# Kernel tuning notes

Hardware: AMD Instinct MI355X
Metric: run time of the kernel (lower is better)

Reference implementation:

```python
import jax, jax.numpy as jnp
import numpy as np

D, H, KVH, HD, FF = 768, 12, 4, 64, 2048
N_REP = H // KVH
EPS = 1e-6


def rmsnorm(x, w):
    # Faithful to source: norm = ||x|| * n^{-1/2}; eps added to norm (not inside sqrt)
    norm = jnp.sqrt(jnp.sum(x * x, axis=-1, keepdims=True)) * (x.shape[-1] ** -0.5)
    return w * x / (norm + EPS)


def rope_tables(seq_len, head_dim, base=10000.0):
    inv_freq = 1.0 / (base ** (np.arange(0, head_dim, 2, dtype=np.float32) / head_dim))
    t = np.arange(seq_len, dtype=np.float32)
    freqs = np.einsum('i,j->ij', t, inv_freq)  # [S, HD/2]
    emb = np.concatenate([freqs, freqs], axis=-1)  # [S, HD]
    return jnp.asarray(np.cos(emb)), jnp.asarray(np.sin(emb))


def rotate_half(x):
    h = x.shape[-1] // 2
    return jnp.concatenate([-x[..., h:], x[..., :h]], axis=-1)


def setup_inputs() -> dict:
    key = jax.random.key(0)
    ks = jax.random.split(key, 9)
    s = 0.02
    return {
        'x': jax.random.normal(ks[0], (2, 2048, D), jnp.float32),
        'Wq': jax.random.normal(ks[1], (H * HD, D), jnp.float32) * s,
        'Wk': jax.random.normal(ks[2], (KVH * HD, D), jnp.float32) * s,
        'Wv': jax.random.normal(ks[3], (KVH * HD, D), jnp.float32) * s,
        'Wo': jax.random.normal(ks[4], (D, H * HD), jnp.float32) * s,
        'Wgate': jax.random.normal(ks[5], (FF, D), jnp.float32) * s,
        'Wup': jax.random.normal(ks[6], (FF, D), jnp.float32) * s,
        'Wdown': jax.random.normal(ks[7], (D, FF), jnp.float32) * s,
        'g1': jnp.ones((D,), jnp.float32),
        'g2': jnp.ones((D,), jnp.float32),
    }


def reference(x, Wq, Wk, Wv, Wo, Wgate, Wup, Wdown, g1, g2):
    B, S, _ = x.shape
    # ---- attention sublayer (pre-norm) ----
    xn = rmsnorm(x, g1)
    q = (xn @ Wq.T).reshape(B, S, H, HD).transpose(0, 2, 1, 3)      # [B,H,S,HD]
    k = (xn @ Wk.T).reshape(B, S, KVH, HD).transpose(0, 2, 1, 3)    # [B,KVH,S,HD]
    v = (xn @ Wv.T).reshape(B, S, KVH, HD).transpose(0, 2, 1, 3)
    cos, sin = rope_tables(S, HD)                                   # [S,HD]
    q = q * cos + rotate_half(q) * sin
    k = k * cos + rotate_half(k) * sin
    # repeat kv heads to match q heads
    k = jnp.repeat(k, N_REP, axis=1)                                # [B,H,S,HD]
    v = jnp.repeat(v, N_REP, axis=1)
    scores = jnp.einsum('bhqd,bhkd->bhqk', q, k) / jnp.sqrt(jnp.float32(HD))
    causal = jnp.tril(jnp.ones((S, S), bool))
    scores = jnp.where(causal, scores, jnp.finfo(scores.dtype).min)
    attn = jax.nn.softmax(scores, axis=-1)
    out = jnp.einsum('bhqk,bhkd->bhqd', attn, v)                    # [B,H,S,HD]
    out = out.transpose(0, 2, 1, 3).reshape(B, S, H * HD) @ Wo.T
    x = x + out
    # ---- SwiGLU FFN sublayer (pre-norm) ----
    xn2 = rmsnorm(x, g2)
    ff = (jax.nn.silu(xn2 @ Wgate.T) * (xn2 @ Wup.T)) @ Wdown.T
    return x + ff
```

## Files before the change

### kernel.cpp

```cpp
#include <hip/hip_runtime.h>
#include <hip/hip_bf16.h>
#include <math.h>

typedef __bf16 bf16;
typedef __attribute__((ext_vector_type(8))) __bf16 bf16x8;
typedef __attribute__((ext_vector_type(4))) __bf16 bf16x4;
typedef __attribute__((ext_vector_type(4))) float f32x4;

#define MFMA16(a,b,c) __builtin_amdgcn_mfma_f32_16x16x32_bf16(a,b,c,0,0,0)

#define BATCH 2
#define SEQ   2048
#define DMODEL 768
#define NH    12
#define NKV   4
#define NREP  3
#define HD    64
#define FFDIM 2048
#define ROWS  (BATCH*SEQ)

#define QSCALE 0.18033688011112042f
#define LOG2E  1.4426950408889634f

#define WB(N) asm volatile("s_waitcnt vmcnt(" #N ")\n\ts_barrier" ::: "memory")
#define BAR() asm volatile("s_barrier" ::: "memory")

__device__ __forceinline__ void gl2lds16(const bf16* g, bf16* l) {
  __builtin_amdgcn_global_load_lds(
      (const __attribute__((address_space(1))) void*)g,
      (__attribute__((address_space(3))) void*)l, 16, 0, 0);
}

struct Cvt7 { const float* s[7]; bf16* d[7]; int n[7]; };
__global__ __launch_bounds__(256) void cvt_all_kernel(Cvt7 c) {
  int seg = blockIdx.y;
  const float* __restrict__ src = c.s[seg];
  bf16* __restrict__ dst = c.d[seg];
  int n = c.n[seg];
  int stride = gridDim.x * 256;
  for (int i = blockIdx.x * 256 + threadIdx.x; i < n; i += stride)
    dst[i] = (bf16)src[i];
}

__global__ __launch_bounds__(256) void rope_tab_kernel(float* __restrict__ tab) {
  int id = blockIdx.x * 256 + threadIdx.x;
  int j = id >> 11, s = id & 2047;
  float inv = expf(-(float)j * (9.210340371976184f / 32.0f));
  float ang = (float)s * inv;
  tab[id] = cosf(ang);
  tab[65536 + id] = sinf(ang);
}

__global__ __launch_bounds__(192) void rmsnorm_kernel(const float* __restrict__ x,
    const float* __restrict__ g, bf16* __restrict__ out) {
  int row = blockIdx.x;
  const float* xr = x + (size_t)row * DMODEL;
  int t = threadIdx.x;
  f32x4 v = *(const f32x4*)(xr + t * 4);
  float ss = v[0] * v[0] + v[1] * v[1] + v[2] * v[2] + v[3] * v[3];
  #pragma unroll
  for (int off = 32; off; off >>= 1) ss += __shfl_xor(ss, off, 64);
  __shared__ float red[3];
  if ((t & 63) == 0) red[t >> 6] = ss;
  __syncthreads();
  float total = red[0] + red[1] + red[2];
  float norm = sqrtf(total) * 0.03608439182435161f;
  float sc = 1.0f / (norm + 1e-6f);
  f32x4 gv = *(const f32x4*)(g + t * 4);
  bf16x4 o;
  #pragma unroll
  for (int i = 0; i < 4; ++i) o[i] = (bf16)(gv[i] * v[i] * sc);
  *(bf16x4*)(out + (size_t)row * DMODEL + t * 4) = o;
}

__global__ __launch_bounds__(256) void gemm_pipe64_kernel(const bf16* __restrict__ A,
    const bf16* __restrict__ B, float* __restrict__ C, const float* __restrict__ R,
    int N, int K) {
  __shared__ __align__(16) bf16 At[4][64 * 32];
  __shared__ __align__(16) bf16 Bt[4][64 * 32];
  int t = threadIdx.x, lane = t & 63, wave = t >> 6;
  int l15 = lane & 15, lq = lane >> 4;
  int wrow = (wave >> 1) * 32, wcol = (wave & 1) * 32;
  int row0 = blockIdx.y * 64, col0 = blockIdx.x * 64;
  const bf16* Ag = A + (size_t)(row0 + (t >> 2)) * K + (t & 3) * 8;
  const bf16* Bg = B + (size_t)(col0 + (t >> 2)) * K + (t & 3) * 8;
  const int NS = K / 32;

  #pragma unroll
  for (int s = 0; s < 4; ++s) {
    int ks = s * 32;
    gl2lds16(Ag + ks, At[s] + t * 8);
    gl2lds16(Bg + ks, Bt[s] + t * 8);
  }

  f32x4 zero = {0.f, 0.f, 0.f, 0.f};
  f32x4 acc[2][2];
  #pragma unroll
  for (int m = 0; m < 2; ++m)
    #pragma unroll
    for (int n = 0; n < 2; ++n) acc[m][n] = zero;

  #define GP_COMPUTE(slot) do {                                              \
    const bf16* at = At[slot]; const bf16* bt = Bt[slot];                    \
    bf16x8 af[2], bfr[2];                                                    \
    _Pragma("unroll")                                                        \
    for (int m = 0; m < 2; ++m)                                              \
      af[m] = *(const bf16x8*)(at + (wrow + m * 16 + l15) * 32 + lq * 8);    \
    _Pragma("unroll")                                                        \
    for (int n = 0; n < 2; ++n)                                              \
      bfr[n] = *(const bf16x8*)(bt + (wcol + n * 16 + l15) * 32 + lq * 8);   \
    _Pragma("unroll")                                                        \
    for (int m = 0; m < 2; ++m)                                              \
      _Pragma("unroll")                                                      \
      for (int n = 0; n < 2; ++n)                                            \
        acc[m][n] = MFMA16(af[m], bfr[n], acc[m][n]);                        \
  } while (0)

  for (int k = 0; k < NS - 3; ++k) {
    WB(6);
    GP_COMPUTE(k & 3);
    BAR();
    if (k <= NS - 5) {
      int ks = (k + 4) * 32;
      gl2lds16(Ag + ks, At[k & 3] + t * 8);
      gl2lds16(Bg + ks, Bt[k & 3] + t * 8);
    }
  }
  for (int k = NS - 3; k < NS; ++k) {
    WB(0);
    GP_COMPUTE(k & 3);
  }
  #undef GP_COMPUTE

  #pragma unroll
  for (int m = 0; m < 2; ++m)
    #pragma unroll
    for (int n = 0; n < 2; ++n)
      #pragma unroll
      for (int r = 0; r < 4; ++r) {
        size_t idx = (size_t)(row0 + wrow + m * 16 + lq * 4 + r) * N
                   + (col0 + wcol + n * 16 + l15);
        C[idx] = acc[m][n][r] + R[idx];
      }
}

__global__ __launch_bounds__(256) void gemm_qkv_kernel(const bf16* __restrict__ A,
    const bf16* __restrict__ Wcat, const float* __restrict__ tab,
    bf16* __restrict__ Qh, bf16* __restrict__ Kh, bf16* __restrict__ Vt) {
  __shared__ __align__(16) bf16 At[4][64 * 32];
  __shared__ __align__(16) bf16 Bt[4][128 * 32];
  const int K = DMODEL;
  int t = threadIdx.x, lane = t & 63, wave = t >> 6;
  int l15 = lane & 15, lq = lane >> 4;
  int wrow = (wave >> 1) * 32, wcol = (wave & 1) * 64;
  int row0 = blockIdx.y * 64, col0 = blockIdx.x * 128;
  const bf16* Ag  = A + (size_t)(row0 + (t >> 2)) * K + (t & 3) * 8;
  const bf16* Bg0 = Wcat + (size_t)(col0 + (t >> 2)) * K + (t & 3) * 8;
  const bf16* Bg1 = Bg0 + (size_t)64 * K;
  const int NS = K / 32;

  #pragma unroll
  for (int s = 0; s < 4; ++s) {
    int ks = s * 32;
    gl2lds16(Ag + ks,  At[s] + t * 8);
    gl2lds16(Bg0 + ks, Bt[s] + t * 8);
    gl2lds16(Bg1 + ks, Bt[s] + 2048 + t * 8);
  }

  f32x4 zero = {0.f, 0.f, 0.f, 0.f};
  f32x4 acc[2][4];
  #pragma unroll
  for (int m = 0; m < 2; ++m)
    #pragma unroll
    for (int n = 0; n < 4; ++n) acc[m][n] = zero;

  #define QK_COMPUTE(slot) do {                                              \
    const bf16* at = At[slot]; const bf16* bt = Bt[slot];                    \
    bf16x8 af[2], bfr[4];                                                    \
    _Pragma("unroll")                                                        \
    for (int m = 0; m < 2; ++m)                                              \
      af[m] = *(const bf16x8*)(at + (wrow + m * 16 + l15) * 32 + lq * 8);    \
    _Pragma("unroll")                                                        \
    for (int n = 0; n < 4; ++n)                                              \
      bfr[n] = *(const bf16x8*)(bt + (wcol + n * 16 + l15) * 32 + lq * 8);   \
    _Pragma("unroll")                                                        \
    for (int m = 0; m < 2; ++m)                                              \
      _Pragma("unroll")                                                      \
      for (int n = 0; n < 4; ++n)                                            \
        acc[m][n] = MFMA16(af[m], bfr[n], acc[m][n]);                        \
  } while (0)

  for (int k = 0; k < NS - 3; ++k) {
    WB(9);
    QK_COMPUTE(k & 3);
    BAR();
    if (k <= NS - 5) {
      int ks = (k + 4) * 32;
      gl2lds16(Ag + ks,  At[k & 3] + t * 8);
      gl2lds16(Bg0 + ks, Bt[k & 3] + t * 8);
      gl2lds16(Bg1 + ks, Bt[k & 3] + 2048 + t * 8);
    }
  }
  for (int k = NS - 3; k < NS; ++k) {
    WB(0);
    QK_COMPUTE(k & 3);
  }
  #undef QK_COMPUTE

  int b = row0 >> 11;
  int s0 = (row0 & 2047) + wrow + lq * 4;
  int colw = col0 + wcol;
  if (colw < 768) {
    int h = colw >> 6;
    f32x4 cv[2][2], sv[2][2];
    #pragma unroll
    for (int m = 0; m < 2; ++m)
      #pragma unroll
      for (int jh = 0; jh < 2; ++jh) {
        const float* cp = tab + (jh * 16 + l15) * 2048 + s0 + m * 16;
        cv[m][jh] = *(const f32x4*)cp;
        sv[m][jh] = *(const f32x4*)(cp + 65536);
      }
    #pragma unroll
    for (int m = 0; m < 2; ++m)
      #pragma unroll
      for (int n = 0; n < 4; ++n) {
        float sgn = (n < 2) ? -1.f : 1.f;
        #pragma unroll
        for (int r = 0; r < 4; ++r) {
          float c = cv[m][n & 1][r], si = sv[m][n & 1][r];
          float rp = (acc[m][n][r] * c + sgn * acc[m][n ^ 2][r] * si) * QSCALE;
          Qh[((size_t)(b * NH + h) * SEQ + s0 + m * 16 + r) * 64 + n * 16 + l15] = (bf16)rp;
        }
      }
  } else if (colw < 1024) {
    int kh = (colw - 768) >> 6;
    f32x4 cv[2][2], sv[2][2];
    #pragma unroll
    for (int m = 0; m < 2; ++m)
      #pragma unroll
      for (int jh = 0; jh < 2; ++jh) {
        const float* cp = tab + (jh * 16 + l15) * 2048 + s0 + m * 16;
        cv[m][jh] = *(const f32x4*)cp;
        sv[m][jh] = *(const f32x4*)(cp + 65536);
      }
    #pragma unroll
    for (int m = 0; m < 2; ++m)
      #pragma unroll
      for (int n = 0; n < 4; ++n) {
        float sgn = (n < 2) ? -1.f : 1.f;
        #pragma unroll
        for (int r = 0; r < 4; ++r) {
          float c = cv[m][n & 1][r], si = sv[m][n & 1][r];
          float rp = acc[m][n][r] * c + sgn * acc[m][n ^ 2][r] * si;
          Kh[((size_t)(b * NKV + kh) * SEQ + s0 + m * 16 + r) * 64 + n * 16 + l15] = (bf16)rp;
        }
      }
  } else {
    int vh = (colw - 1024) >> 6;
    #pragma unroll
    for (int m = 0; m < 2; ++m)
      #pragma unroll
      for (int n = 0; n < 4; ++n) {
        bf16x4 pv;
        #pragma unroll
        for (int r = 0; r < 4; ++r) pv[r] = (bf16)acc[m][n][r];
        *(bf16x4*)(Vt + ((size_t)(b * NKV + vh) * 64 + n * 16 + l15) * SEQ + s0 + m * 16) = pv;
      }
  }
}

__global__ __launch_bounds__(256) void gemm_gu_kernel(const bf16* __restrict__ A,
    const bf16* __restrict__ Wg, const bf16* __restrict__ Wu, bf16* __restrict__ H) {
  __shared__ __align__(16) bf16 At[3][128 * 32];
  __shared__ __align__(16) bf16 Bgt[3][64 * 32];
  __shared__ __align__(16) bf16 But[3][64 * 32];
  const int K = DMODEL;
  int t = threadIdx.x, lane = t & 63, wave = t >> 6;
  int l15 = lane & 15, lq = lane >> 4;
  int wrow = (wave >> 1) * 64, wcol = (wave & 1) * 32;
  int row0 = blockIdx.y * 128, col0 = blockIdx.x * 64;
  const bf16* Ag0 = A + (size_t)(row0 + (t >> 2)) * K + (t & 3) * 8;
  const bf16* Ag1 = Ag0 + (size_t)64 * K;
  const bf16* Gg  = Wg + (size_t)(col0 + (t >> 2)) * K + (t & 3) * 8;
  const bf16* Ug  = Wu + (size_t)(col0 + (t >> 2)) * K + (t & 3) * 8;
  const int NS = K / 32;

  #pragma unroll
  for (int s = 0; s < 3; ++s) {
    int ks = s * 32;
    gl2lds16(Ag0 + ks, At[s] + t * 8);
    gl2lds16(Ag1 + ks, At[s] + 2048 + t * 8);
    gl2lds16(Gg + ks,  Bgt[s] + t * 8);
    gl2lds16(Ug + ks,  But[s] + t * 8);
  }

  f32x4 zero = {0.f, 0.f, 0.f, 0.f};
  f32x4 ag[4][2], au[4][2];
  #pragma unroll
  for (int m = 0; m < 4; ++m)
    #pragma unroll
    for (int n = 0; n < 2; ++n) { ag[m][n] = zero; au[m][n] = zero; }

  #define GU_COMPUTE(slot) do {                                              \
    const bf16* at = At[slot];                                               \
    const bf16* bgt = Bgt[slot]; const bf16* but = But[slot];                \
    bf16x8 af[4], bg[2], bu[2];                                              \
    _Pragma("unroll")                                                        \
    for (int m = 0; m < 4; ++m)                                              \
      af[m] = *(const bf16x8*)(at + (wrow + m * 16 + l15) * 32 + lq * 8);    \
    _Pragma("unroll")                                                        \
    for (int n = 0; n < 2; ++n) {                                            \
      bg[n] = *(const bf16x8*)(bgt + (wcol + n * 16 + l15) * 32 + lq * 8);   \
      bu[n] = *(const bf16x8*)(but + (wcol + n * 16 + l15) * 32 + lq * 8);   \
    }                                                                        \
    _Pragma("unroll")                                                        \
    for (int m = 0; m < 4; ++m)                                              \
      _Pragma("unroll")                                                      \
      for (int n = 0; n < 2; ++n) {                                          \
        ag[m][n] = MFMA16(af[m], bg[n], ag[m][n]);                           \
        au[m][n] = MFMA16(af[m], bu[n], au[m][n]);                           \
      }                                                                      \
  } while (0)

  int slot = 0;
  for (int k = 0; k < NS - 2; ++k) {
    WB(8);
    GU_COMPUTE(slot);
    BAR();
    if (k <= NS - 4) {
      int ks = (k + 3) * 32;
      gl2lds16(Ag0 + ks, At[slot] + t * 8);
      gl2lds16(Ag1 + ks, At[slot] + 2048 + t * 8);
      gl2lds16(Gg + ks,  Bgt[slot] + t * 8);
      gl2lds16(Ug + ks,  But[slot] + t * 8);
    }
    slot = (slot == 2) ? 0 : slot + 1;
  }
  for (int k = NS - 2; k < NS; ++k) {
    WB(0);
    GU_COMPUTE(slot);
    slot = (slot == 2) ? 0 : slot + 1;
  }
  #undef GU_COMPUTE

  #pragma unroll
  for (int m = 0; m < 4; ++m)
    #pragma unroll
    for (int n = 0; n < 2; ++n)
      #pragma unroll
      for (int r = 0; r < 4; ++r) {
        int row = row0 + wrow + m * 16 + lq * 4 + r;
        int col = col0 + wcol + n * 16 + l15;
        float g = ag[m][n][r], u = au[m][n][r];
        float sg = g / (1.f + __builtin_amdgcn_exp2f(-g * LOG2E));
        H[(size_t)row * FFDIM + col] = (bf16)(sg * u);
      }
}

__global__ __launch_bounds__(256) void attn_kernel(const bf16* __restrict__ Qh,
    const bf16* __restrict__ Kh, const bf16* __restrict__ Vt, bf16* __restrict__ out) {
  __shared__ __align__(16) bf16 Kl0[2][64 * 32];
  __shared__ __align__(16) bf16 Kl1[2][64 * 32];
  __shared__ __align__(16) bf16 Vl0[2][64 * 32];
  __shared__ __align__(16) bf16 Vl1[2][64 * 32];
  __shared__ __align__(16) bf16 P[4][16 * 80];

  int idx = blockIdx.x;
  int qt = 31 - (idx / 24);
  int bh = idx % 24;
  int q0blk = qt * 64;
  int b = bh / NH, h = bh % NH;
  int kvh = h / NREP;
  int t = threadIdx.x;
  int lane = t & 63, wave = t >> 6;
  int l15 = lane & 15, lq = lane >> 4;
  int qw = q0blk + wave * 16;
  const bf16* Qb = Qh + (size_t)(b * NH + h) * SEQ * 64;
  const bf16* Kb = Kh + (size_t)(b * NKV + kvh) * SEQ * 64;
  const bf16* Vb = Vt + (size_t)(b * NKV + kvh) * 64 * SEQ;

  bf16x8 bq0 = *(const bf16x8*)(Qb + (size_t)(qw + l15) * 64 + lq * 8);
  bf16x8 bq1 = *(const bf16x8*)(Qb + (size_t)(qw + l15) * 64 + 32 + lq * 8);

  const bf16* Kg = Kb + (size_t)(t >> 2) * 64 + (t & 3) * 8;
  const bf16* Vg = Vb + (size_t)(t >> 2) * SEQ + (t & 3) * 8;
  bf16* Pw = P[wave];
  int Pwq = l15 * 80, lq8 = lq * 8, lq4 = lq * 4;
  const int NS = qt + 1;

  #pragma unroll
  for (int s = 0; s < 2; ++s) {
    int ks = (s < NS ? s : NS - 1) * 64;
    gl2lds16(Kg + (size_t)ks * 64,      Kl0[s] + t * 8);
    gl2lds16(Kg + (size_t)ks * 64 + 32, Kl1[s] + t * 8);
    gl2lds16(Vg + ks,                   Vl0[s] + t * 8);
    gl2lds16(Vg + ks + 32,              Vl1[s] + t * 8);
  }

  f32x4 zero = {0.f, 0.f, 0.f, 0.f};
  f32x4 o[4];
  o[0] = zero; o[1] = zero; o[2] = zero; o[3] = zero;
  float l_r = 0.f;

  #define ATTN_STEP(kk, slot) do {                                           \
    int k0 = (kk) * 64;                                                      \
    const bf16* kl0 = Kl0[slot]; const bf16* kl1 = Kl1[slot];                \
    const bf16* vl0 = Vl0[slot]; const bf16* vl1 = Vl1[slot];                \
    f32x4 s[4];                                                              \
    _Pragma("unroll")                                                        \
    for (int c = 0; c < 4; ++c) {                                            \
      bf16x8 ak0 = *(const bf16x8*)(kl0 + (c * 16 + l15) * 32 + lq8);        \
      bf16x8 ak1 = *(const bf16x8*)(kl1 + (c * 16 + l15) * 32 + lq8);        \
      s[c] = zero;                                                           \
      s[c] = MFMA16(ak0, bq0, s[c]);                                         \
      s[c] = MFMA16(ak1, bq1, s[c]);                                         \
    }                                                                        \
    if (k0 + 63 > qw) {                                                      \
      int qmk = qw + l15 - k0 - lq4;                                         \
      _Pragma("unroll")                                                      \
      for (int c = 0; c < 4; ++c)                                            \
        _Pragma("unroll")                                                    \
        for (int r = 0; r < 4; ++r)                                          \
          if (c * 16 + r > qmk) s[c][r] = -INFINITY;                         \
    }                                                                        \
    _Pragma("unroll")                                                        \
    for (int c = 0; c < 4; ++c) {                                            \
      bf16x4 pe;                                                             \
      _Pragma("unroll")                                                      \
      for (int r = 0; r < 4; ++r) {                                          \
        float e = __builtin_amdgcn_exp2f(s[c][r]);                           \
        l_r += e;                                                            \
        pe[r] = (bf16)e;                                                     \
      }                                                                      \
      *(bf16x4*)(Pw + Pwq + c * 16 + lq4) = pe;                              \
    }                                                                        \
    bf16x8 bp0 = *(const bf16x8*)(Pw + Pwq + lq8);                           \
    bf16x8 bp1 = *(const bf16x8*)(Pw + Pwq + 32 + lq8);                      \
    _Pragma("unroll")                                                        \
    for (int n = 0; n < 4; ++n) {                                            \
      bf16x8 av0 = *(const bf16x8*)(vl0 + (n * 16 + l15) * 32 + lq8);        \
      bf16x8 av1 = *(const bf16x8*)(vl1 + (n * 16 + l15) * 32 + lq8);        \
      o[n] = MFMA16(av0, bp0, o[n]);                                         \
      o[n] = MFMA16(av1, bp1, o[n]);                                         \
    }                                                                        \
  } while (0)

  for (int k = 0; k < NS - 1; ++k) {
    WB(4);
    ATTN_STEP(k, k & 1);
    BAR();
    if (k <= NS - 3) {
      int ks = (k + 2) * 64;
      gl2lds16(Kg + (size_t)ks * 64,      Kl0[k & 1] + t * 8);
      gl2lds16(Kg + (size_t)ks * 64 + 32, Kl1[k & 1] + t * 8);
      gl2lds16(Vg + ks,                   Vl0[k & 1] + t * 8);
      gl2lds16(Vg + ks + 32,              Vl1[k & 1] + t * 8);
    }
  }
  {
    WB(0);
    ATTN_STEP(NS - 1, (NS - 1) & 1);
  }
  #undef ATTN_STEP

  float lt = l_r;
  lt += __shfl_xor(lt, 16, 64);
  lt += __shfl_xor(lt, 32, 64);
  float inv = 1.f / lt;
  int q = qw + l15;
  bf16* orow = out + (size_t)(b * SEQ + q) * DMODEL + h * 64;
  #pragma unroll
  for (int n = 0; n < 4; ++n) {
    bf16x4 po;
    #pragma unroll
    for (int r = 0; r < 4; ++r) po[r] = (bf16)(o[n][r] * inv);
    *(bf16x4*)(orow + n * 16 + lq4) = po;
  }
}

extern "C" void kernel_launch(void* const* d_in, const int* in_sizes, int n_in,
                              void* d_out, int out_size, void* d_ws, size_t ws_size,
                              hipStream_t stream) {
  const float* x     = (const float*)d_in[0];
  const float* Wq    = (const float*)d_in[1];
  const float* Wk    = (const float*)d_in[2];
  const float* Wv    = (const float*)d_in[3];
  const float* Wo    = (const float*)d_in[4];
  const float* Wgate = (const float*)d_in[5];
  const float* Wup   = (const float*)d_in[6];
  const float* Wdown = (const float*)d_in[7];
  const float* g1    = (const float*)d_in[8];
  const float* g2    = (const float*)d_in[9];
  float* out = (float*)d_out;

  char* ws = (char*)d_ws;
  size_t off = 0;
  auto alloc = [&](size_t bytes) { size_t o = off; off += (bytes + 255) & ~(size_t)255; return o; };
  size_t o_tab  = alloc((size_t)2 * 32 * 2048 * 4);
  size_t o_x1   = alloc((size_t)4096 * 768 * 4);
  size_t o_xn   = alloc((size_t)4096 * 768 * 2);
  size_t o_Qh   = alloc((size_t)2 * 12 * 2048 * 64 * 2);
  size_t o_Kh   = alloc((size_t)2 * 4 * 2048 * 64 * 2);
  size_t o_Vt   = alloc((size_t)2 * 4 * 64 * 2048 * 2);
  size_t o_ao   = alloc((size_t)4096 * 768 * 2);
  size_t o_H    = alloc((size_t)4096 * 2048 * 2);
  size_t o_Wcat = alloc((size_t)1280 * 768 * 2);
  size_t o_Wo   = alloc((size_t)768 * 768 * 2);
  size_t o_Wgu  = alloc((size_t)4096 * 768 * 2);
  size_t o_Wdn  = alloc((size_t)768 * 2048 * 2);
  if (ws_size < off) return;

  float* tab  = (float*)(ws + o_tab);
  float* fx1  = (float*)(ws + o_x1);
  bf16* bxn   = (bf16*)(ws + o_xn);
  bf16* bQh   = (bf16*)(ws + o_Qh);
  bf16* bKh   = (bf16*)(ws + o_Kh);
  bf16* bVt   = (bf16*)(ws + o_Vt);
  bf16* bao   = (bf16*)(ws + o_ao);
  bf16* bH    = (bf16*)(ws + o_H);
  bf16* bWcat = (bf16*)(ws + o_Wcat);
  bf16* bWo   = (bf16*)(ws + o_Wo);
  bf16* bWgu  = (bf16*)(ws + o_Wgu);
  bf16* bWdn  = (bf16*)(ws + o_Wdn);

  rope_tab_kernel<<<256, 256, 0, stream>>>(tab);

  Cvt7 c;
  c.s[0] = Wq;    c.d[0] = bWcat;              c.n[0] = 768 * 768;
  c.s[1] = Wk;    c.d[1] = bWcat + 768 * 768;  c.n[1] = 256 * 768;
  c.s[2] = Wv;    c.d[2] = bWcat + 1024 * 768; c.n[2] = 256 * 768;
  c.s[3] = Wo;    c.d[3] = bWo;                c.n[3] = 768 * 768;
  c.s[4] = Wgate; c.d[4] = bWgu;               c.n[4] = 2048 * 768;
  c.s[5] = Wup;   c.d[5] = bWgu + 2048 * 768;  c.n[5] = 2048 * 768;
  c.s[6] = Wdown; c.d[6] = bWdn;               c.n[6] = 768 * 2048;
  cvt_all_kernel<<<dim3(256, 7), 256, 0, stream>>>(c);

  rmsnorm_kernel<<<4096, 192, 0, stream>>>(x, g1, bxn);
  gemm_qkv_kernel<<<dim3(10, 64), 256, 0, stream>>>(bxn, bWcat, tab, bQh, bKh, bVt);
  attn_kernel<<<dim3(768), 256, 0, stream>>>(bQh, bKh, bVt, bao);
  gemm_pipe64_kernel<<<dim3(12, 64), 256, 0, stream>>>(bao, bWo, fx1, x, 768, 768);

  rmsnorm_kernel<<<4096, 192, 0, stream>>>(fx1, g2, bxn);
  gemm_gu_kernel<<<dim3(32, 32), 256, 0, stream>>>(bxn, bWgu, bWgu + 2048 * 768, bH);
  gemm_pipe64_kernel<<<dim3(12, 64), 256, 0, stream>>>(bH, bWdn, out, fx1, 768, 2048);
}
```

Before: 255.0 us.

## Prefetch before compute to drop a barrier, enlarge gate/up tile, vectorize weight cast

The GEMM main loops now issue the next stage's global-to-LDS loads right after the wait/barrier, into the slot freed in the previous iteration, before computing. This removes the second barrier per k-step, with prefetch depth adjusted to match. The gate/up GEMM tile grows from 128x64 to 128x128 per block, with 2-stage lookahead and 2 blocks per CU requested, improving operand reuse at the cost of more registers and LDS. The fp32-to-bf16 weight conversion now uses 4-wide vector loads and stores.

```diff
diff --git a/kernel.cpp b/kernel.cpp
--- a/kernel.cpp
+++ b/kernel.cpp
@@ -36,10 +36,15 @@
   int seg = blockIdx.y;
   const float* __restrict__ src = c.s[seg];
   bf16* __restrict__ dst = c.d[seg];
-  int n = c.n[seg];
+  int n4 = c.n[seg] >> 2;
   int stride = gridDim.x * 256;
-  for (int i = blockIdx.x * 256 + threadIdx.x; i < n; i += stride)
-    dst[i] = (bf16)src[i];
+  for (int i = blockIdx.x * 256 + threadIdx.x; i < n4; i += stride) {
+    f32x4 v = ((const f32x4*)src)[i];
+    bf16x4 o;
+    #pragma unroll
+    for (int j = 0; j < 4; ++j) o[j] = (bf16)v[j];
+    ((bf16x4*)dst)[i] = o;
+  }
 }
 
 __global__ __launch_bounds__(256) void rope_tab_kernel(float* __restrict__ tab) {
@@ -87,7 +92,7 @@
   const int NS = K / 32;
 
   #pragma unroll
-  for (int s = 0; s < 4; ++s) {
+  for (int s = 0; s < 3; ++s) {
     int ks = s * 32;
     gl2lds16(Ag + ks, At[s] + t * 8);
     gl2lds16(Bg + ks, Bt[s] + t * 8);
@@ -117,14 +122,11 @@
   } while (0)
 
   for (int k = 0; k < NS - 3; ++k) {
-    WB(6);
+    WB(4);
+    int ks = (k + 3) * 32;
+    gl2lds16(Ag + ks, At[(k + 3) & 3] + t * 8);
+    gl2lds16(Bg + ks, Bt[(k + 3) & 3] + t * 8);
     GP_COMPUTE(k & 3);
-    BAR();
-    if (k <= NS - 5) {
-      int ks = (k + 4) * 32;
-      gl2lds16(Ag + ks, At[k & 3] + t * 8);
-      gl2lds16(Bg + ks, Bt[k & 3] + t * 8);
-    }
   }
   for (int k = NS - 3; k < NS; ++k) {
     WB(0);
@@ -160,7 +162,7 @@
   const int NS = K / 32;
 
   #pragma unroll
-  for (int s = 0; s < 4; ++s) {
+  for (int s = 0; s < 3; ++s) {
     int ks = s * 32;
     gl2lds16(Ag + ks,  At[s] + t * 8);
     gl2lds16(Bg0 + ks, Bt[s] + t * 8);
@@ -191,15 +193,12 @@
   } while (0)
 
   for (int k = 0; k < NS - 3; ++k) {
-    WB(9);
+    WB(6);
+    int ks = (k + 3) * 32;
+    gl2lds16(Ag + ks,  At[(k + 3) & 3] + t * 8);
+    gl2lds16(Bg0 + ks, Bt[(k + 3) & 3] + t * 8);
+    gl2lds16(Bg1 + ks, Bt[(k + 3) & 3] + 2048 + t * 8);
     QK_COMPUTE(k & 3);
-    BAR();
-    if (k <= NS - 5) {
-      int ks = (k + 4) * 32;
-      gl2lds16(Ag + ks,  At[k & 3] + t * 8);
-      gl2lds16(Bg0 + ks, Bt[k & 3] + t * 8);
-      gl2lds16(Bg1 + ks, Bt[k & 3] + 2048 + t * 8);
-    }
   }
   for (int k = NS - 3; k < NS; ++k) {
     WB(0);
@@ -270,84 +269,88 @@
   }
 }
 
-__global__ __launch_bounds__(256) void gemm_gu_kernel(const bf16* __restrict__ A,
+__global__ __launch_bounds__(256, 2) void gemm_gu_kernel(const bf16* __restrict__ A,
     const bf16* __restrict__ Wg, const bf16* __restrict__ Wu, bf16* __restrict__ H) {
   __shared__ __align__(16) bf16 At[3][128 * 32];
-  __shared__ __align__(16) bf16 Bgt[3][64 * 32];
-  __shared__ __align__(16) bf16 But[3][64 * 32];
+  __shared__ __align__(16) bf16 Bgt[3][128 * 32];
+  __shared__ __align__(16) bf16 But[3][128 * 32];
   const int K = DMODEL;
   int t = threadIdx.x, lane = t & 63, wave = t >> 6;
   int l15 = lane & 15, lq = lane >> 4;
-  int wrow = (wave >> 1) * 64, wcol = (wave & 1) * 32;
-  int row0 = blockIdx.y * 128, col0 = blockIdx.x * 64;
+  int wrow = (wave >> 1) * 64, wcol = (wave & 1) * 64;
+  int row0 = blockIdx.y * 128, col0 = blockIdx.x * 128;
   const bf16* Ag0 = A + (size_t)(row0 + (t >> 2)) * K + (t & 3) * 8;
   const bf16* Ag1 = Ag0 + (size_t)64 * K;
-  const bf16* Gg  = Wg + (size_t)(col0 + (t >> 2)) * K + (t & 3) * 8;
-  const bf16* Ug  = Wu + (size_t)(col0 + (t >> 2)) * K + (t & 3) * 8;
+  const bf16* Gg0 = Wg + (size_t)(col0 + (t >> 2)) * K + (t & 3) * 8;
+  const bf16* Gg1 = Gg0 + (size_t)64 * K;
+  const bf16* Ug0 = Wu + (size_t)(col0 + (t >> 2)) * K + (t & 3) * 8;
+  const bf16* Ug1 = Ug0 + (size_t)64 * K;
   const int NS = K / 32;
 
   #pragma unroll
-  for (int s = 0; s < 3; ++s) {
+  for (int s = 0; s < 2; ++s) {
     int ks = s * 32;
     gl2lds16(Ag0 + ks, At[s] + t * 8);
     gl2lds16(Ag1 + ks, At[s] + 2048 + t * 8);
-    gl2lds16(Gg + ks,  Bgt[s] + t * 8);
-    gl2lds16(Ug + ks,  But[s] + t * 8);
+    gl2lds16(Gg0 + ks, Bgt[s] + t * 8);
+    gl2lds16(Gg1 + ks, Bgt[s] + 2048 + t * 8);
+    gl2lds16(Ug0 + ks, But[s] + t * 8);
+    gl2lds16(Ug1 + ks, But[s] + 2048 + t * 8);
   }
 
   f32x4 zero = {0.f, 0.f, 0.f, 0.f};
-  f32x4 ag[4][2], au[4][2];
+  f32x4 ag[4][4], au[4][4];
   #pragma unroll
   for (int m = 0; m < 4; ++m)
     #pragma unroll
-    for (int n = 0; n < 2; ++n) { ag[m][n] = zero; au[m][n] = zero; }
+    for (int n = 0; n < 4; ++n) { ag[m][n] = zero; au[m][n] = zero; }
 
   #define GU_COMPUTE(slot) do {                                              \
     const bf16* at = At[slot];                                               \
     const bf16* bgt = Bgt[slot]; const bf16* but = But[slot];                \
-    bf16x8 af[4], bg[2], bu[2];                                              \
+    bf16x8 af[4], bg[4], bu[4];                                              \
     _Pragma("unroll")                                                        \
     for (int m = 0; m < 4; ++m)                                              \
       af[m] = *(const bf16x8*)(at + (wrow + m * 16 + l15) * 32 + lq * 8);    \
     _Pragma("unroll")                                                        \
-    for (int n = 0; n < 2; ++n) {                                            \
+    for (int n = 0; n < 4; ++n) {                                            \
       bg[n] = *(const bf16x8*)(bgt + (wcol + n * 16 + l15) * 32 + lq * 8);   \
       bu[n] = *(const bf16x8*)(but + (wcol + n * 16 + l15) * 32 + lq * 8);   \
     }                                                                        \
     _Pragma("unroll")                                                        \
     for (int m = 0; m < 4; ++m)                                              \
       _Pragma("unroll")                                                      \
-      for (int n = 0; n < 2; ++n) {                                          \
+      for (int n = 0; n < 4; ++n) {                                          \
         ag[m][n] = MFMA16(af[m], bg[n], ag[m][n]);                           \
         au[m][n] = MFMA16(af[m], bu[n], au[m][n]);                           \
       }                                                                      \
   } while (0)
 
-  int slot = 0;
+  int sc = 0, sw = 2;
   for (int k = 0; k < NS - 2; ++k) {
-    WB(8);
-    GU_COMPUTE(slot);
-    BAR();
-    if (k <= NS - 4) {
-      int ks = (k + 3) * 32;
-      gl2lds16(Ag0 + ks, At[slot] + t * 8);
-      gl2lds16(Ag1 + ks, At[slot] + 2048 + t * 8);
-      gl2lds16(Gg + ks,  Bgt[slot] + t * 8);
-      gl2lds16(Ug + ks,  But[slot] + t * 8);
-    }
-    slot = (slot == 2) ? 0 : slot + 1;
+    WB(6);
+    int ks = (k + 2) * 32;
+    gl2lds16(Ag0 + ks, At[sw] + t * 8);
+    gl2lds16(Ag1 + ks, At[sw] + 2048 + t * 8);
+    gl2lds16(Gg0 + ks, Bgt[sw] + t * 8);
+    gl2lds16(Gg1 + ks, Bgt[sw] + 2048 + t * 8);
+    gl2lds16(Ug0 + ks, But[sw] + t * 8);
+    gl2lds16(Ug1 + ks, But[sw] + 2048 + t * 8);
+    GU_COMPUTE(sc);
+    sc = (sc == 2) ? 0 : sc + 1;
+    sw = (sw == 2) ? 0 : sw + 1;
   }
   for (int k = NS - 2; k < NS; ++k) {
     WB(0);
-    GU_COMPUTE(slot);
-    slot = (slot == 2) ? 0 : slot + 1;
+    GU_COMPUTE(sc);
+    sc = (sc == 2) ? 0 : sc + 1;
   }
   #undef GU_COMPUTE
 
   #pragma unroll
   for (int m = 0; m < 4; ++m)
     #pragma unroll
-    for (int n = 0; n < 2; ++n)
+    for (int n = 0; n < 4; ++n)
       #pragma unroll
       for (int r = 0; r < 4; ++r) {
         int row = row0 + wrow + m * 16 + lq * 4 + r;
@@ -542,6 +545,6 @@
   gemm_pipe64_kernel<<<dim3(12, 64), 256, 0, stream>>>(bao, bWo, fx1, x, 768, 768);
 
   rmsnorm_kernel<<<4096, 192, 0, stream>>>(fx1, g2, bxn);
-  gemm_gu_kernel<<<dim3(32, 32), 256, 0, stream>>>(bxn, bWgu, bWgu + 2048 * 768, bH);
+  gemm_gu_kernel<<<dim3(16, 32), 256, 0, stream>>>(bxn, bWgu, bWgu + 2048 * 768, bH);
   gemm_pipe64_kernel<<<dim3(12, 64), 256, 0, stream>>>(bH, bWdn, out, fx1, 768, 2048);
 }
```

Result: no change. 256.6 us (+0.6%).
